# Performance work log

Hardware: AMD Instinct MI355X
Metric: run time of the kernel (lower is better)

## Reference

```python
import jax, jax.numpy as jnp
import numpy as np

WIN = 9
EPS = 1e-05


def _box_sum(x, win=WIN):
    # Separable 3D box-filter sum: mathematically identical to conv3d with a
    pad = win // 2
    for axis in range(3):  # spatial axes D, H, W
        kshape = [1, 1, 1]
        kshape[axis] = win
        filt = jnp.ones((1, 1, *kshape), dtype=x.dtype)  # OIDHW
        padding = [(pad, pad) if i == axis else (0, 0) for i in range(3)]
        x = jax.lax.conv_general_dilated(
            x, filt, window_strides=(1, 1, 1), padding=padding,
            dimension_numbers=('NCDHW', 'OIDHW', 'NCDHW'))
    return x


def setup_inputs() -> dict:
    key = jax.random.key(0)
    k1, k2 = jax.random.split(key)
    shape = (2, 1, 160, 192, 224)
    y_true = jax.random.uniform(k1, shape, dtype=jnp.float32)
    y_pred = jax.random.uniform(k2, shape, dtype=jnp.float32)
    return {"y_true": y_true, "y_pred": y_pred}


def reference(y_true, y_pred):
    ii, ji = y_true, y_pred
    win_size = jnp.asarray(float(WIN ** 3), dtype=ii.dtype)

    i_sum = _box_sum(ii)
    j_sum = _box_sum(ji)
    i2_sum = _box_sum(ii * ii)
    j2_sum = _box_sum(ji * ji)
    ij_sum = _box_sum(ii * ji)

    ui = i_sum / win_size
    uj = j_sum / win_size
    cross = ij_sum - uj * i_sum - ui * j_sum + ui * uj * win_size
    i_var = jnp.maximum(i2_sum - 2 * ui * i_sum + ui * ui * win_size, EPS)
    j_var = jnp.maximum(j2_sum - 2 * uj * j_sum + uj * uj * win_size, EPS)
    return -jnp.mean(cross * cross / (i_var * j_var))
```

## Files before the change

kernel.cpp:

```cpp
#include <hip/hip_runtime.h>

namespace {

constexpr int BD = 2;
constexpr int DD = 160, HH = 192, WW = 224;
constexpr float INV_WIN = 1.0f / 729.0f;
constexpr float EPSV = 1e-5f;

constexpr int TH = 16, TW = 16;
constexpr int DC = 16;
constexpr int NREAL = DC + 8;
constexpr int NSS = NREAL / 2;
constexpr int NCH = DD / DC;
constexpr int GX = WW / TW;
constexpr int GY = HH / TH;
constexpr int GZ = BD * NCH;
constexpr int NBLK = GX * GY * GZ;
constexpr double NTOT = (double)BD * DD * HH * WW;

constexpr int SR_RS = 20;
constexpr int SR_FS = 488;
constexpr int SR_PL = 5 * SR_FS;
constexpr int SC_RS = 20;
constexpr int SC_FS = 328;
constexpr int SC_PL = 5 * SC_FS;

}

__device__ __forceinline__ float4 f4add(float4 a, float4 b) {
  return make_float4(a.x + b.x, a.y + b.y, a.z + b.z, a.w + b.w);
}
__device__ __forceinline__ float4 f4sub(float4 a, float4 b) {
  return make_float4(a.x - b.x, a.y - b.y, a.z - b.z, a.w - b.w);
}

__global__ __launch_bounds__(256)
void ncc_fused(const float* __restrict__ x, const float* __restrict__ y,
               float* __restrict__ bsum) {
  const int tid = threadIdx.x;
  const int w0 = blockIdx.x * TW;
  const int h0 = blockIdx.y * TH;
  const int zb = blockIdx.z;
  const int b  = zb / NCH;
  const int d0 = (zb - b * NCH) * DC;

  __shared__ __align__(16) float srowF[2 * SR_PL];
  __shared__ __align__(16) float scolF[2 * SC_PL];
  __shared__ float swsum[4];

  const bool s2a = tid < 192;
  const int p2  = tid / 96;
  const int t96 = tid - p2 * 96;
  const int r2  = t96 >> 2;
  const int seg = tid & 3;
  const int gh  = h0 - 4 + r2;
  const int gw0 = w0 - 4 + seg * 4;
  const bool hok = (unsigned)gh < (unsigned)HH;
  const bool fastw = (gw0 >= 0) && (gw0 + 11 < WW);
  const unsigned plane = (unsigned)HH * WW;

  auto prefetch = [&](int s, float4* vx, float4* vy) {
    const int din = d0 - 4 + s;
    const float4 z = make_float4(0.f, 0.f, 0.f, 0.f);
    vx[0] = vx[1] = vx[2] = z;
    vy[0] = vy[1] = vy[2] = z;
    if (s2a && hok && (s < NREAL) && (din >= 0) && (din < DD)) {
      const unsigned rb = ((unsigned)b * DD + (unsigned)din) * plane + (unsigned)gh * WW;
      if (fastw) {
        const float4* px = (const float4*)(x + rb + gw0);
        const float4* py = (const float4*)(y + rb + gw0);
        vx[0] = px[0]; vx[1] = px[1]; vx[2] = px[2];
        vy[0] = py[0]; vy[1] = py[1]; vy[2] = py[2];
      } else {
        float* fx = (float*)vx;
        float* fy = (float*)vy;
#pragma unroll
        for (int e = 0; e < 12; ++e) {
          const int gw = gw0 + e;
          if ((unsigned)gw < (unsigned)WW) {
            fx[e] = x[rb + gw];
            fy[e] = y[rb + gw];
          }
        }
      }
    }
  };

  const int ow = tid & 15;
  const int oh = tid >> 4;

  float rg0[9], rg1[9], rg2[9], rg3[9], rg4[9];
#pragma unroll
  for (int k = 0; k < 9; ++k) { rg0[k]=0.f; rg1[k]=0.f; rg2[k]=0.f; rg3[k]=0.f; rg4[k]=0.f; }
  float a0=0.f, a1=0.f, a2=0.f, a3=0.f, a4=0.f;
  float lsum = 0.0f;

  float4 px4[3], py4[3];
  prefetch(p2, px4, py4);

#pragma unroll
  for (int ss = 0; ss < NSS; ++ss) {
    const int sA = 2 * ss;
    const int sB = 2 * ss + 1;
    const int slA = sA % 9;
    const int slB = sB % 9;

    float4 nx4[3], ny4[3];
    prefetch(2 * (ss + 1) + p2, nx4, ny4);

    if (s2a) {
      float xv[12], yv[12];
#pragma unroll
      for (int k = 0; k < 3; ++k) {
        *(float4*)&xv[4 * k] = px4[k];
        *(float4*)&yv[4 * k] = py4[k];
      }
      float s0=0.f, s1=0.f, s2=0.f, s3=0.f, s4=0.f;
#pragma unroll
      for (int k = 0; k < 9; ++k) {
        s0 += xv[k]; s1 += yv[k];
        s2 = fmaf(xv[k], xv[k], s2);
        s3 = fmaf(yv[k], yv[k], s3);
        s4 = fmaf(xv[k], yv[k], s4);
      }
      float o0[4], o1[4], o2[4], o3[4], o4[4];
      o0[0]=s0; o1[0]=s1; o2[0]=s2; o3[0]=s3; o4[0]=s4;
#pragma unroll
      for (int t = 0; t < 3; ++t) {
        const float xn = xv[9 + t], xo = xv[t];
        const float yn = yv[9 + t], yo = yv[t];
        s0 += xn - xo;
        s1 += yn - yo;
        s2 += fmaf(xn, xn, -(xo * xo));
        s3 += fmaf(yn, yn, -(yo * yo));
        s4 += fmaf(xn, yn, -(xo * yo));
        o0[t+1]=s0; o1[t+1]=s1; o2[t+1]=s2; o3[t+1]=s3; o4[t+1]=s4;
      }
      const int rb = p2 * SR_PL + r2 * SR_RS + seg * 4;
      *(float4*)&srowF[rb + 0 * SR_FS] = make_float4(o0[0], o0[1], o0[2], o0[3]);
      *(float4*)&srowF[rb + 1 * SR_FS] = make_float4(o1[0], o1[1], o1[2], o1[3]);
      *(float4*)&srowF[rb + 2 * SR_FS] = make_float4(o2[0], o2[1], o2[2], o2[3]);
      *(float4*)&srowF[rb + 3 * SR_FS] = make_float4(o3[0], o3[1], o3[2], o3[3]);
      *(float4*)&srowF[rb + 4 * SR_FS] = make_float4(o4[0], o4[1], o4[2], o4[3]);
    }
    __syncthreads();

    if (tid < 160) {
      const int p3  = tid / 80;
      const int r3  = tid - p3 * 80;
      const int q   = r3 / 20;
      const int rem = r3 - q * 20;
      const int f3  = rem >> 2;
      const int w43 = rem & 3;
      const int o0q = q * 4;
      const float* rp = &srowF[p3 * SR_PL + f3 * SR_FS + w43 * 4];
      float4 keep[4];
      float4 s = make_float4(0.f, 0.f, 0.f, 0.f);
#pragma unroll
      for (int t = 0; t < 8; ++t) {
        const float4 v = *(const float4*)&rp[(o0q + t) * SR_RS];
        if (t < 4) keep[t] = v;
        s = f4add(s, v);
      }
      float* cp = &scolF[p3 * SC_PL + f3 * SC_FS + w43 * 4];
#pragma unroll
      for (int t = 0; t < 4; ++t) {
        const int o = o0q + t;
        s = f4add(s, *(const float4*)&rp[(o + 8) * SR_RS]);
        *(float4*)&cp[o * SC_RS] = s;
        s = f4sub(s, keep[t]);
      }
    }
    __syncthreads();

    const float* cA = &scolF[oh * SC_RS + ow];
    const float* cB = cA + SC_PL;
    const float gA0=cA[0*SC_FS], gA1=cA[1*SC_FS], gA2=cA[2*SC_FS],
                gA3=cA[3*SC_FS], gA4=cA[4*SC_FS];
    const float gB0=cB[0*SC_FS], gB1=cB[1*SC_FS], gB2=cB[2*SC_FS],
                gB3=cB[3*SC_FS], gB4=cB[4*SC_FS];

    a0 += gA0 - rg0[slA]; rg0[slA] = gA0;
    a1 += gA1 - rg1[slA]; rg1[slA] = gA1;
    a2 += gA2 - rg2[slA]; rg2[slA] = gA2;
    a3 += gA3 - rg3[slA]; rg3[slA] = gA3;
    a4 += gA4 - rg4[slA]; rg4[slA] = gA4;
    if (sA >= 8) {
      const float cross = fmaf(-a0 * INV_WIN, a1, a4);
      const float iv = fmaxf(fmaf(-a0 * INV_WIN, a0, a2), EPSV);
      const float jv = fmaxf(fmaf(-a1 * INV_WIN, a1, a3), EPSV);
      lsum += (cross * cross) / (iv * jv);
    }
    a0 += gB0 - rg0[slB]; rg0[slB] = gB0;
    a1 += gB1 - rg1[slB]; rg1[slB] = gB1;
    a2 += gB2 - rg2[slB]; rg2[slB] = gB2;
    a3 += gB3 - rg3[slB]; rg3[slB] = gB3;
    a4 += gB4 - rg4[slB]; rg4[slB] = gB4;
    if (sB >= 8) {
      const float cross = fmaf(-a0 * INV_WIN, a1, a4);
      const float iv = fmaxf(fmaf(-a0 * INV_WIN, a0, a2), EPSV);
      const float jv = fmaxf(fmaf(-a1 * INV_WIN, a1, a3), EPSV);
      lsum += (cross * cross) / (iv * jv);
    }

#pragma unroll
    for (int k = 0; k < 3; ++k) { px4[k] = nx4[k]; py4[k] = ny4[k]; }
  }

#pragma unroll
  for (int off = 32; off > 0; off >>= 1) lsum += __shfl_down(lsum, off);
  if ((tid & 63) == 0) swsum[tid >> 6] = lsum;
  __syncthreads();
  if (tid == 0) {
    const int bid = ((int)blockIdx.z * GY + (int)blockIdx.y) * GX + (int)blockIdx.x;
    bsum[bid] = swsum[0] + swsum[1] + swsum[2] + swsum[3];
  }
}

__global__ __launch_bounds__(256)
void ncc_finalize(const float* __restrict__ bsum, float* __restrict__ out) {
  double s = 0.0;
  for (int i = threadIdx.x; i < NBLK; i += 256) s += (double)bsum[i];
#pragma unroll
  for (int off = 32; off > 0; off >>= 1) s += __shfl_down(s, off);
  __shared__ double sh[4];
  if ((threadIdx.x & 63) == 0) sh[threadIdx.x >> 6] = s;
  __syncthreads();
  if (threadIdx.x == 0)
    out[0] = (float)(-(sh[0] + sh[1] + sh[2] + sh[3]) / NTOT);
}

extern "C" void kernel_launch(void* const* d_in, const int* in_sizes, int n_in,
                              void* d_out, int out_size, void* d_ws, size_t ws_size,
                              hipStream_t stream) {
  const float* x = (const float*)d_in[0];
  const float* y = (const float*)d_in[1];
  float* bsum = (float*)d_ws;
  float* out  = (float*)d_out;

  dim3 grid(GX, GY, GZ);
  ncc_fused<<<grid, dim3(256), 0, stream>>>(x, y, bsum);
  ncc_finalize<<<1, dim3(256), 0, stream>>>(bsum, out);
}
```

Baseline: 228.1 us.

## Restructure W/H box-sum stages with per-column thread mapping and drop register prefetch

Each thread of the first stage now handles one W column position across 4 consecutive H rows, computing the full 9-wide W sum directly with unaligned vector loads instead of a sliding 4-output window. The shared-memory layout is transposed so the H stage reads 24 contiguous values per column and runs a sliding sum over 16 outputs. The software prefetch of the next depth slice into registers is removed and loads are issued inline. This aims to simplify indexing and cut shared-memory traffic, but it does more redundant W-direction arithmetic and loses the load/compute overlap that the prefetch provided.

```diff
diff --git a/kernel.cpp b/kernel.cpp
--- a/kernel.cpp
+++ b/kernel.cpp
@@ -18,21 +18,14 @@
 constexpr int NBLK = GX * GY * GZ;
 constexpr double NTOT = (double)BD * DD * HH * WW;
 
-constexpr int SR_RS = 20;
-constexpr int SR_FS = 488;
+constexpr int SR_FS = 388;
 constexpr int SR_PL = 5 * SR_FS;
-constexpr int SC_RS = 20;
-constexpr int SC_FS = 328;
+constexpr int SC_FS = 324;
 constexpr int SC_PL = 5 * SC_FS;
 
 }
 
-__device__ __forceinline__ float4 f4add(float4 a, float4 b) {
-  return make_float4(a.x + b.x, a.y + b.y, a.z + b.z, a.w + b.w);
-}
-__device__ __forceinline__ float4 f4sub(float4 a, float4 b) {
-  return make_float4(a.x - b.x, a.y - b.y, a.z - b.z, a.w - b.w);
-}
+typedef float f4u __attribute__((ext_vector_type(4), aligned(4)));
 
 __global__ __launch_bounds__(256)
 void ncc_fused(const float* __restrict__ x, const float* __restrict__ y,
@@ -50,41 +43,20 @@
 
   const bool s2a = tid < 192;
   const int p2  = tid / 96;
-  const int t96 = tid - p2 * 96;
-  const int r2  = t96 >> 2;
-  const int seg = tid & 3;
-  const int gh  = h0 - 4 + r2;
-  const int gw0 = w0 - 4 + seg * 4;
-  const bool hok = (unsigned)gh < (unsigned)HH;
-  const bool fastw = (gw0 >= 0) && (gw0 + 11 < WW);
+  const int t96 = tid - 96 * p2;
+  const int rq  = t96 >> 4;
+  const int wl  = t96 & 15;
+  const int gwb = w0 + wl - 4;
+  const bool fastw = (gwb >= 0) && (gwb + 8 < WW);
+  const int gh0 = h0 - 4 + rq * 4;
+  int roff[4]; bool rok[4];
+#pragma unroll
+  for (int k = 0; k < 4; ++k) {
+    const int gh = gh0 + k;
+    rok[k]  = (unsigned)gh < (unsigned)HH;
+    roff[k] = gh * WW + gwb;
+  }
   const unsigned plane = (unsigned)HH * WW;
-
-  auto prefetch = [&](int s, float4* vx, float4* vy) {
-    const int din = d0 - 4 + s;
-    const float4 z = make_float4(0.f, 0.f, 0.f, 0.f);
-    vx[0] = vx[1] = vx[2] = z;
-    vy[0] = vy[1] = vy[2] = z;
-    if (s2a && hok && (s < NREAL) && (din >= 0) && (din < DD)) {
-      const unsigned rb = ((unsigned)b * DD + (unsigned)din) * plane + (unsigned)gh * WW;
-      if (fastw) {
-        const float4* px = (const float4*)(x + rb + gw0);
-        const float4* py = (const float4*)(y + rb + gw0);
-        vx[0] = px[0]; vx[1] = px[1]; vx[2] = px[2];
-        vy[0] = py[0]; vy[1] = py[1]; vy[2] = py[2];
-      } else {
-        float* fx = (float*)vx;
-        float* fy = (float*)vy;
-#pragma unroll
-        for (int e = 0; e < 12; ++e) {
-          const int gw = gw0 + e;
-          if ((unsigned)gw < (unsigned)WW) {
-            fx[e] = x[rb + gw];
-            fy[e] = y[rb + gw];
-          }
-        }
-      }
-    }
-  };
 
   const int ow = tid & 15;
   const int oh = tid >> 4;
@@ -95,90 +67,94 @@
   float a0=0.f, a1=0.f, a2=0.f, a3=0.f, a4=0.f;
   float lsum = 0.0f;
 
-  float4 px4[3], py4[3];
-  prefetch(p2, px4, py4);
-
 #pragma unroll
   for (int ss = 0; ss < NSS; ++ss) {
     const int sA = 2 * ss;
-    const int sB = 2 * ss + 1;
+    const int sB = sA + 1;
     const int slA = sA % 9;
     const int slB = sB % 9;
 
-    float4 nx4[3], ny4[3];
-    prefetch(2 * (ss + 1) + p2, nx4, ny4);
-
     if (s2a) {
-      float xv[12], yv[12];
-#pragma unroll
-      for (int k = 0; k < 3; ++k) {
-        *(float4*)&xv[4 * k] = px4[k];
-        *(float4*)&yv[4 * k] = py4[k];
+      const int s   = sA + p2;
+      const int din = d0 - 4 + s;
+      const bool dok = (din >= 0) && (din < DD);
+      const float* xp = x + (size_t)((unsigned)b * DD + (unsigned)(dok ? din : 0)) * plane;
+      const float* yp = y + (size_t)((unsigned)b * DD + (unsigned)(dok ? din : 0)) * plane;
+      float q0[4], q1[4], q2[4], q3[4], q4[4];
+#pragma unroll
+      for (int k = 0; k < 4; ++k) {
+        float xv[9], yv[9];
+        const bool ok = dok && rok[k];
+        if (ok && fastw) {
+          const float* px = xp + roff[k];
+          const float* py = yp + roff[k];
+          const f4u xa = *(const f4u*)px;
+          const f4u xb = *(const f4u*)(px + 4);
+          const f4u ya = *(const f4u*)py;
+          const f4u yb = *(const f4u*)(py + 4);
+#pragma unroll
+          for (int e = 0; e < 4; ++e) { xv[e] = xa[e]; xv[e+4] = xb[e]; yv[e] = ya[e]; yv[e+4] = yb[e]; }
+          xv[8] = px[8]; yv[8] = py[8];
+        } else if (ok) {
+#pragma unroll
+          for (int e = 0; e < 9; ++e) {
+            const int gw = gwb + e;
+            const bool in = (unsigned)gw < (unsigned)WW;
+            xv[e] = in ? xp[roff[k] + e] : 0.0f;
+            yv[e] = in ? yp[roff[k] + e] : 0.0f;
+          }
+        } else {
+#pragma unroll
+          for (int e = 0; e < 9; ++e) { xv[e] = 0.0f; yv[e] = 0.0f; }
+        }
+        float s0=0.f, s1=0.f, s2=0.f, s3=0.f, s4=0.f;
+#pragma unroll
+        for (int t = 0; t < 9; ++t) {
+          s0 += xv[t]; s1 += yv[t];
+          s2 = fmaf(xv[t], xv[t], s2);
+          s3 = fmaf(yv[t], yv[t], s3);
+          s4 = fmaf(xv[t], yv[t], s4);
+        }
+        q0[k]=s0; q1[k]=s1; q2[k]=s2; q3[k]=s3; q4[k]=s4;
       }
-      float s0=0.f, s1=0.f, s2=0.f, s3=0.f, s4=0.f;
-#pragma unroll
-      for (int k = 0; k < 9; ++k) {
-        s0 += xv[k]; s1 += yv[k];
-        s2 = fmaf(xv[k], xv[k], s2);
-        s3 = fmaf(yv[k], yv[k], s3);
-        s4 = fmaf(xv[k], yv[k], s4);
-      }
-      float o0[4], o1[4], o2[4], o3[4], o4[4];
-      o0[0]=s0; o1[0]=s1; o2[0]=s2; o3[0]=s3; o4[0]=s4;
-#pragma unroll
-      for (int t = 0; t < 3; ++t) {
-        const float xn = xv[9 + t], xo = xv[t];
-        const float yn = yv[9 + t], yo = yv[t];
-        s0 += xn - xo;
-        s1 += yn - yo;
-        s2 += fmaf(xn, xn, -(xo * xo));
-        s3 += fmaf(yn, yn, -(yo * yo));
-        s4 += fmaf(xn, yn, -(xo * yo));
-        o0[t+1]=s0; o1[t+1]=s1; o2[t+1]=s2; o3[t+1]=s3; o4[t+1]=s4;
-      }
-      const int rb = p2 * SR_PL + r2 * SR_RS + seg * 4;
-      *(float4*)&srowF[rb + 0 * SR_FS] = make_float4(o0[0], o0[1], o0[2], o0[3]);
-      *(float4*)&srowF[rb + 1 * SR_FS] = make_float4(o1[0], o1[1], o1[2], o1[3]);
-      *(float4*)&srowF[rb + 2 * SR_FS] = make_float4(o2[0], o2[1], o2[2], o2[3]);
-      *(float4*)&srowF[rb + 3 * SR_FS] = make_float4(o3[0], o3[1], o3[2], o3[3]);
-      *(float4*)&srowF[rb + 4 * SR_FS] = make_float4(o4[0], o4[1], o4[2], o4[3]);
+      const int wb = p2 * SR_PL + wl * 24 + rq * 4;
+      *(float4*)&srowF[wb + 0 * SR_FS] = make_float4(q0[0], q0[1], q0[2], q0[3]);
+      *(float4*)&srowF[wb + 1 * SR_FS] = make_float4(q1[0], q1[1], q1[2], q1[3]);
+      *(float4*)&srowF[wb + 2 * SR_FS] = make_float4(q2[0], q2[1], q2[2], q2[3]);
+      *(float4*)&srowF[wb + 3 * SR_FS] = make_float4(q3[0], q3[1], q3[2], q3[3]);
+      *(float4*)&srowF[wb + 4 * SR_FS] = make_float4(q4[0], q4[1], q4[2], q4[3]);
     }
     __syncthreads();
 
     if (tid < 160) {
       const int p3  = tid / 80;
-      const int r3  = tid - p3 * 80;
-      const int q   = r3 / 20;
-      const int rem = r3 - q * 20;
-      const int f3  = rem >> 2;
-      const int w43 = rem & 3;
-      const int o0q = q * 4;
-      const float* rp = &srowF[p3 * SR_PL + f3 * SR_FS + w43 * 4];
-      float4 keep[4];
-      float4 s = make_float4(0.f, 0.f, 0.f, 0.f);
-#pragma unroll
-      for (int t = 0; t < 8; ++t) {
-        const float4 v = *(const float4*)&rp[(o0q + t) * SR_RS];
-        if (t < 4) keep[t] = v;
-        s = f4add(s, v);
-      }
-      float* cp = &scolF[p3 * SC_PL + f3 * SC_FS + w43 * 4];
-#pragma unroll
-      for (int t = 0; t < 4; ++t) {
-        const int o = o0q + t;
-        s = f4add(s, *(const float4*)&rp[(o + 8) * SR_RS]);
-        *(float4*)&cp[o * SC_RS] = s;
-        s = f4sub(s, keep[t]);
-      }
+      const int r3  = tid - 80 * p3;
+      const int f3  = r3 >> 4;
+      const int wl3 = r3 & 15;
+      const float* rp = &srowF[p3 * SR_PL + f3 * SR_FS + wl3 * 24];
+      float rv[24];
+#pragma unroll
+      for (int t = 0; t < 6; ++t) *(float4*)&rv[4 * t] = *(const float4*)&rp[4 * t];
+      float acc = rv[0];
+#pragma unroll
+      for (int t = 1; t < 9; ++t) acc += rv[t];
+      float ov[16];
+      ov[0] = acc;
+#pragma unroll
+      for (int o = 1; o < 16; ++o) { acc += rv[o + 8] - rv[o - 1]; ov[o] = acc; }
+      float* cp = &scolF[p3 * SC_PL + f3 * SC_FS + wl3 * 20];
+#pragma unroll
+      for (int t = 0; t < 4; ++t)
+        *(float4*)&cp[4 * t] = make_float4(ov[4*t], ov[4*t+1], ov[4*t+2], ov[4*t+3]);
     }
     __syncthreads();
 
-    const float* cA = &scolF[oh * SC_RS + ow];
+    const float* cA = &scolF[ow * 20 + oh];
     const float* cB = cA + SC_PL;
-    const float gA0=cA[0*SC_FS], gA1=cA[1*SC_FS], gA2=cA[2*SC_FS],
-                gA3=cA[3*SC_FS], gA4=cA[4*SC_FS];
-    const float gB0=cB[0*SC_FS], gB1=cB[1*SC_FS], gB2=cB[2*SC_FS],
-                gB3=cB[3*SC_FS], gB4=cB[4*SC_FS];
+    const float gA0 = cA[0*SC_FS], gA1 = cA[1*SC_FS], gA2 = cA[2*SC_FS],
+                gA3 = cA[3*SC_FS], gA4 = cA[4*SC_FS];
+    const float gB0 = cB[0*SC_FS], gB1 = cB[1*SC_FS], gB2 = cB[2*SC_FS],
+                gB3 = cB[3*SC_FS], gB4 = cB[4*SC_FS];
 
     a0 += gA0 - rg0[slA]; rg0[slA] = gA0;
     a1 += gA1 - rg1[slA]; rg1[slA] = gA1;
@@ -202,9 +178,6 @@
       const float jv = fmaxf(fmaf(-a1 * INV_WIN, a1, a3), EPSV);
       lsum += (cross * cross) / (iv * jv);
     }
-
-#pragma unroll
-    for (int k = 0; k < 3; ++k) { px4[k] = nx4[k]; py4[k] = ny4[k]; }
   }
 
 #pragma unroll
```

Measured after the change: 351.5 us. 54.1% more time.

## Transpose shared-memory staging so H-pass reads contiguous column vectors

Applied to the files above, without the earlier changes.

The W-pass results are now written to shared memory transposed (w-major with h contiguous, stride 28), so each H-pass thread owns one w column and reads its 24 h values with six float4 loads, then does a full 16-output sliding sum in registers. The column buffer is likewise stored w-major with h contiguous, and the final gather indexes it transposed. This replaces many strided float4 loads and the keep/subtract scheme, cutting LDS instruction count, but the W-pass now issues scalar LDS stores and the 160 active threads each do more serial adds, with possible bank conflicts from the new strides.

```diff
diff --git a/kernel.cpp b/kernel.cpp
--- a/kernel.cpp
+++ b/kernel.cpp
@@ -18,20 +18,11 @@
 constexpr int NBLK = GX * GY * GZ;
 constexpr double NTOT = (double)BD * DD * HH * WW;
 
-constexpr int SR_RS = 20;
-constexpr int SR_FS = 488;
-constexpr int SR_PL = 5 * SR_FS;
-constexpr int SC_RS = 20;
-constexpr int SC_FS = 328;
-constexpr int SC_PL = 5 * SC_FS;
-
-}
-
-__device__ __forceinline__ float4 f4add(float4 a, float4 b) {
-  return make_float4(a.x + b.x, a.y + b.y, a.z + b.z, a.w + b.w);
-}
-__device__ __forceinline__ float4 f4sub(float4 a, float4 b) {
-  return make_float4(a.x - b.x, a.y - b.y, a.z - b.z, a.w - b.w);
+constexpr int SR_FS = 452;
+constexpr int SR_PL = 2280;
+constexpr int SC_FS = 324;
+constexpr int SC_PL = 1620;
+
 }
 
 __global__ __launch_bounds__(256)
@@ -50,7 +41,7 @@
 
   const bool s2a = tid < 192;
   const int p2  = tid / 96;
-  const int t96 = tid - p2 * 96;
+  const int t96 = tid - 96 * p2;
   const int r2  = t96 >> 2;
   const int seg = tid & 3;
   const int gh  = h0 - 4 + r2;
@@ -101,7 +92,7 @@
 #pragma unroll
   for (int ss = 0; ss < NSS; ++ss) {
     const int sA = 2 * ss;
-    const int sB = 2 * ss + 1;
+    const int sB = sA + 1;
     const int slA = sA % 9;
     const int slB = sB % 9;
 
@@ -123,62 +114,54 @@
         s3 = fmaf(yv[k], yv[k], s3);
         s4 = fmaf(xv[k], yv[k], s4);
       }
-      float o0[4], o1[4], o2[4], o3[4], o4[4];
-      o0[0]=s0; o1[0]=s1; o2[0]=s2; o3[0]=s3; o4[0]=s4;
-#pragma unroll
-      for (int t = 0; t < 3; ++t) {
-        const float xn = xv[9 + t], xo = xv[t];
-        const float yn = yv[9 + t], yo = yv[t];
+      float* wb = &srowF[p2 * SR_PL + (seg * 4) * 28 + r2];
+      wb[0 * SR_FS] = s0; wb[1 * SR_FS] = s1; wb[2 * SR_FS] = s2;
+      wb[3 * SR_FS] = s3; wb[4 * SR_FS] = s4;
+#pragma unroll
+      for (int t = 1; t < 4; ++t) {
+        const float xn = xv[8 + t], xo = xv[t - 1];
+        const float yn = yv[8 + t], yo = yv[t - 1];
         s0 += xn - xo;
         s1 += yn - yo;
         s2 += fmaf(xn, xn, -(xo * xo));
         s3 += fmaf(yn, yn, -(yo * yo));
         s4 += fmaf(xn, yn, -(xo * yo));
-        o0[t+1]=s0; o1[t+1]=s1; o2[t+1]=s2; o3[t+1]=s3; o4[t+1]=s4;
-      }
-      const int rb = p2 * SR_PL + r2 * SR_RS + seg * 4;
-      *(float4*)&srowF[rb + 0 * SR_FS] = make_float4(o0[0], o0[1], o0[2], o0[3]);
-      *(float4*)&srowF[rb + 1 * SR_FS] = make_float4(o1[0], o1[1], o1[2], o1[3]);
-      *(float4*)&srowF[rb + 2 * SR_FS] = make_float4(o2[0], o2[1], o2[2], o2[3]);
-      *(float4*)&srowF[rb + 3 * SR_FS] = make_float4(o3[0], o3[1], o3[2], o3[3]);
-      *(float4*)&srowF[rb + 4 * SR_FS] = make_float4(o4[0], o4[1], o4[2], o4[3]);
+        float* wt = wb + t * 28;
+        wt[0 * SR_FS] = s0; wt[1 * SR_FS] = s1; wt[2 * SR_FS] = s2;
+        wt[3 * SR_FS] = s3; wt[4 * SR_FS] = s4;
+      }
     }
     __syncthreads();
 
     if (tid < 160) {
       const int p3  = tid / 80;
-      const int r3  = tid - p3 * 80;
-      const int q   = r3 / 20;
-      const int rem = r3 - q * 20;
-      const int f3  = rem >> 2;
-      const int w43 = rem & 3;
-      const int o0q = q * 4;
-      const float* rp = &srowF[p3 * SR_PL + f3 * SR_FS + w43 * 4];
-      float4 keep[4];
-      float4 s = make_float4(0.f, 0.f, 0.f, 0.f);
-#pragma unroll
-      for (int t = 0; t < 8; ++t) {
-        const float4 v = *(const float4*)&rp[(o0q + t) * SR_RS];
-        if (t < 4) keep[t] = v;
-        s = f4add(s, v);
-      }
-      float* cp = &scolF[p3 * SC_PL + f3 * SC_FS + w43 * 4];
-#pragma unroll
-      for (int t = 0; t < 4; ++t) {
-        const int o = o0q + t;
-        s = f4add(s, *(const float4*)&rp[(o + 8) * SR_RS]);
-        *(float4*)&cp[o * SC_RS] = s;
-        s = f4sub(s, keep[t]);
-      }
+      const int r3  = tid - 80 * p3;
+      const int f3  = r3 >> 4;
+      const int wl3 = r3 & 15;
+      const float* rp = &srowF[p3 * SR_PL + f3 * SR_FS + wl3 * 28];
+      float rv[24];
+#pragma unroll
+      for (int t = 0; t < 6; ++t) *(float4*)&rv[4 * t] = *(const float4*)&rp[4 * t];
+      float acc = rv[0];
+#pragma unroll
+      for (int t = 1; t < 9; ++t) acc += rv[t];
+      float ov[16];
+      ov[0] = acc;
+#pragma unroll
+      for (int o = 1; o < 16; ++o) { acc += rv[o + 8] - rv[o - 1]; ov[o] = acc; }
+      float* cp = &scolF[p3 * SC_PL + f3 * SC_FS + wl3 * 20];
+#pragma unroll
+      for (int t = 0; t < 4; ++t)
+        *(float4*)&cp[4 * t] = make_float4(ov[4*t], ov[4*t+1], ov[4*t+2], ov[4*t+3]);
     }
     __syncthreads();
 
-    const float* cA = &scolF[oh * SC_RS + ow];
+    const float* cA = &scolF[ow * 20 + oh];
     const float* cB = cA + SC_PL;
-    const float gA0=cA[0*SC_FS], gA1=cA[1*SC_FS], gA2=cA[2*SC_FS],
-                gA3=cA[3*SC_FS], gA4=cA[4*SC_FS];
-    const float gB0=cB[0*SC_FS], gB1=cB[1*SC_FS], gB2=cB[2*SC_FS],
-                gB3=cB[3*SC_FS], gB4=cB[4*SC_FS];
+    const float gA0 = cA[0*SC_FS], gA1 = cA[1*SC_FS], gA2 = cA[2*SC_FS],
+                gA3 = cA[3*SC_FS], gA4 = cA[4*SC_FS];
+    const float gB0 = cB[0*SC_FS], gB1 = cB[1*SC_FS], gB2 = cB[2*SC_FS],
+                gB3 = cB[3*SC_FS], gB4 = cB[4*SC_FS];
 
     a0 += gA0 - rg0[slA]; rg0[slA] = gA0;
     a1 += gA1 - rg1[slA]; rg1[slA] = gA1;
```

Measured after the change: 211.1 us. -7.4%, faster.
